# Optimization experiments

Measured on AMD Instinct MI355X. Metric: run time of the kernel, lower is better.

## Reference

```python
import jax, jax.numpy as jnp
import numpy as np

B, S, H, NH = 1, 4096, 768, 12
D = H // NH  # per-head dim = 64


def setup_inputs() -> dict:
    key = jax.random.key(0)
    ks = jax.random.split(key, 10)
    p = 0.02  # param scale
    return {
        "x": jax.random.normal(ks[0], (B, S, H), jnp.float32),
        "Wq": jax.random.normal(ks[1], (H, H), jnp.float32) * p,
        "bq": jax.random.normal(ks[2], (H,), jnp.float32) * p,
        "Wk": jax.random.normal(ks[3], (H, H), jnp.float32) * p,
        "bk": jax.random.normal(ks[4], (H,), jnp.float32) * p,
        "Wv": jax.random.normal(ks[5], (H, H), jnp.float32) * p,
        "bv": jax.random.normal(ks[6], (H,), jnp.float32) * p,
        "Wo": jax.random.normal(ks[7], (H, H), jnp.float32) * p,
        "bo": jax.random.normal(ks[8], (H,), jnp.float32) * p,
        "attn_mask": jax.random.randint(ks[9], (B, 1, 1, S), 0, 2).astype(bool),
    }


def _split_heads(t):
    # [B, S, H] -> [B, NH, S, D]
    return t.reshape(B, S, NH, D).transpose(0, 2, 1, 3)


def reference(x, Wq, bq, Wk, bk, Wv, bv, Wo, bo, attn_mask):
    q = _split_heads(x @ Wq.T + bq)
    k = _split_heads(x @ Wk.T + bk)
    v = _split_heads(x @ Wv.T + bv)
    scores = jnp.einsum('bhqd,bhkd->bhqk', q, k) / np.sqrt(D).astype(np.float32)
    scores = jnp.where(attn_mask, jnp.float32(-1e9), scores)
    attn = jax.nn.softmax(scores, axis=-1)
    ctx = jnp.einsum('bhqk,bhkd->bhqd', attn, v)
    ctx = ctx.transpose(0, 2, 1, 3).reshape(B, S, H)  # merge heads
    return ctx @ Wo.T + bo
```

## Files before the change

kernel.cpp:

```cpp
#include <hip/hip_runtime.h>
#include <stdint.h>

#define S_LEN 4096
#define HDIM  768
#define NHEAD 12
#define DHEAD 64

typedef _Float16 f16;
typedef __attribute__((ext_vector_type(8)))  _Float16 f16x8;
typedef __attribute__((ext_vector_type(4)))  _Float16 f16x4;
typedef __attribute__((ext_vector_type(4)))  float    f32x4;
typedef __attribute__((ext_vector_type(16))) float    f32x16;

typedef __attribute__((address_space(1))) void gv_t;
typedef __attribute__((address_space(3))) void lv_t;

__device__ __forceinline__ void async_copy16(const void* g, void* l) {
  __builtin_amdgcn_global_load_lds((gv_t*)g, (lv_t*)l, 16, 0, 0);
}

__device__ __forceinline__ float fast_exp2(float x) {
#if __has_builtin(__builtin_amdgcn_exp2f)
  return __builtin_amdgcn_exp2f(x);
#else
  return exp2f(x);
#endif
}

__device__ __forceinline__ int swz4(int row) { return (row ^ (row >> 2)) & 3; }

constexpr size_t OFF_META = 0;
constexpr size_t OFF_RIDX = 256;
constexpr size_t OFF_XB   = 65536;
constexpr size_t SZ_XB    = (size_t)S_LEN * HDIM * 2;
constexpr size_t OFF_WQKV = OFF_XB + SZ_XB;
constexpr size_t SZ_WQKV  = (size_t)3 * HDIM * HDIM * 2;
constexpr size_t OFF_WO   = OFF_WQKV + SZ_WQKV;
constexpr size_t SZ_WO    = (size_t)HDIM * HDIM * 2;
constexpr size_t OFF_Q    = OFF_WO + SZ_WO;
constexpr size_t SZ_HD    = (size_t)NHEAD * S_LEN * DHEAD * 2;
constexpr size_t OFF_K    = OFF_Q + SZ_HD;
constexpr size_t OFF_VT   = OFF_K + SZ_HD;
constexpr size_t OFF_VR   = OFF_VT + SZ_HD;
constexpr size_t OFF_PO1  = OFF_VR + SZ_HD;

__global__ __launch_bounds__(256) void k_prep(const float* __restrict__ x,
                                              const float* __restrict__ wq,
                                              const float* __restrict__ wk,
                                              const float* __restrict__ wv,
                                              const float* __restrict__ wo,
                                              const int* __restrict__ mi,
                                              f16* __restrict__ dst,
                                              int* __restrict__ ridx,
                                              int* __restrict__ meta) {
  __shared__ int s_flag;
  __shared__ int s_cnt[256];
  const int b = blockIdx.x, tid = threadIdx.x;
  if (b < 5376) {
    int i = b * 256 + tid;
    const float* src; int off;
    if (i < 786432) { src = x; off = i; }
    else {
      int j = i - 786432;
      int w = j / 147456;
      off = j - w * 147456;
      src = (w == 0) ? wq : (w == 1) ? wk : (w == 2) ? wv : wo;
    }
    float4 v = ((const float4*)src)[off];
    f16x4 h;
    h[0] = (f16)v.x; h[1] = (f16)v.y; h[2] = (f16)v.z; h[3] = (f16)v.w;
    ((f16x4*)dst)[i] = h;
    return;
  }
  if (tid == 0) s_flag = 1;
  __syncthreads();
  int bad = 0;
  #pragma unroll
  for (int k = 0; k < 4; ++k) {
    int v = mi[k * 256 + tid];
    if (v != 0 && v != 1) bad = 1;
  }
  if (bad) atomicAnd(&s_flag, 0);
  __syncthreads();
  const int isInt = s_flag;
  const unsigned char* mu8 = (const unsigned char*)mi;
  int keep[16]; int cnt = 0;
  const int s0 = tid * 16;
  #pragma unroll
  for (int k = 0; k < 16; ++k) {
    int mval = isInt ? mi[s0 + k] : (int)mu8[s0 + k];
    keep[k] = (mval == 0) ? 1 : 0;
    cnt += keep[k];
    ridx[s0 + k] = 0;
  }
  s_cnt[tid] = cnt;
  __syncthreads();
  for (int off = 1; off < 256; off <<= 1) {
    int t = (tid >= off) ? s_cnt[tid - off] : 0;
    __syncthreads();
    s_cnt[tid] += t;
    __syncthreads();
  }
  int base = s_cnt[tid] - cnt;
  #pragma unroll
  for (int k = 0; k < 16; ++k) {
    if (keep[k]) { ridx[base] = s0 + k; ++base; }
  }
  if (tid == 255) meta[0] = s_cnt[255];
}

__global__ __launch_bounds__(256) void k_qkv(
    const f16* __restrict__ xb, const f16* __restrict__ wqkv,
    const float* __restrict__ bq, const float* __restrict__ bk, const float* __restrict__ bv,
    const int* __restrict__ ridx, const int* __restrict__ meta,
    f16* __restrict__ Qh, f16* __restrict__ Kc, f16* __restrict__ Vrow) {
  __shared__ __attribute__((aligned(16))) f16 lA[128 * 32];
  __shared__ __attribute__((aligned(16))) f16 lB[128 * 32];
  const int tid = threadIdx.x;
  const int wid = tid >> 6, lane = tid & 63;
  const int hf = lane >> 5, l31 = lane & 31;
  const int wm = wid >> 1, wn = wid & 1;
  const int tn = blockIdx.x;
  const int m0 = blockIdx.y * 128;
  const int mat = tn / 6;
  const int nb = (tn % 6) * 128;
  const int kc = meta[0];
  if (mat != 0 && m0 >= kc) return;
  const f16* wbase = wqkv + (size_t)mat * HDIM * HDIM;

  const int ar0 = tid >> 2, ar1 = 64 + (tid >> 2);
  const f16* asrc0;
  const f16* asrc1;
  if (mat == 0) {
    asrc0 = xb + (size_t)(m0 + ar0) * HDIM;
    asrc1 = xb + (size_t)(m0 + ar1) * HDIM;
  } else {
    int g0 = (m0 + ar0 < kc) ? ridx[m0 + ar0] : 0;
    int g1 = (m0 + ar1 < kc) ? ridx[m0 + ar1] : 0;
    asrc0 = xb + (size_t)g0 * HDIM;
    asrc1 = xb + (size_t)g1 * HDIM;
  }
  const int slot = tid & 3;
  const int gs0 = slot ^ swz4(ar0);
  const int gs1 = slot ^ swz4(ar1);

  f32x16 acc[2][2] = {};

  for (int k0 = 0; k0 < HDIM; k0 += 32) {
    async_copy16((const char*)(asrc0 + k0) + gs0 * 16, (char*)lA + (wid * 64) * 16);
    async_copy16((const char*)(asrc1 + k0) + gs1 * 16, (char*)lA + (256 + wid * 64) * 16);
    async_copy16((const char*)(wbase + (size_t)(nb + ar0) * HDIM + k0) + gs0 * 16,
                 (char*)lB + (wid * 64) * 16);
    async_copy16((const char*)(wbase + (size_t)(nb + ar1) * HDIM + k0) + gs1 * 16,
                 (char*)lB + (256 + wid * 64) * 16);
    __syncthreads();
    #pragma unroll
    for (int kk = 0; kk < 2; ++kk) {
      f16x8 af[2], bf[2];
      #pragma unroll
      for (int mi = 0; mi < 2; ++mi) {
        int row = wm * 64 + mi * 32 + l31;
        af[mi] = *(const f16x8*)&lA[row * 32 + (((kk * 2 + hf) ^ swz4(row)) * 8)];
      }
      #pragma unroll
      for (int ni = 0; ni < 2; ++ni) {
        int row = wn * 64 + ni * 32 + l31;
        bf[ni] = *(const f16x8*)&lB[row * 32 + (((kk * 2 + hf) ^ swz4(row)) * 8)];
      }
      #pragma unroll
      for (int mi = 0; mi < 2; ++mi)
        #pragma unroll
        for (int ni = 0; ni < 2; ++ni)
          acc[mi][ni] = __builtin_amdgcn_mfma_f32_32x32x16_f16(af[mi], bf[ni], acc[mi][ni], 0, 0, 0);
    }
    __syncthreads();
  }

  const float* bias = (mat == 0) ? bq : (mat == 1) ? bk : bv;
  const float qscale = 0.125f * 1.44269504088896341f;
  f16* kvdst = (mat == 1) ? Kc : Vrow;
  #pragma unroll
  for (int mi = 0; mi < 2; ++mi) {
    #pragma unroll
    for (int ni = 0; ni < 2; ++ni) {
      int n = nb + wn * 64 + ni * 32 + l31;
      int head = n >> 6, d = n & 63;
      float b = bias[n];
      #pragma unroll
      for (int reg = 0; reg < 16; ++reg) {
        int s = m0 + wm * 64 + mi * 32 + (reg & 3) + 8 * (reg >> 2) + 4 * hf;
        float val = acc[mi][ni][reg] + b;
        if (mat == 0) {
          Qh[((size_t)head * S_LEN + s) * DHEAD + d] = (f16)(val * qscale);
        } else if (s < kc) {
          kvdst[((size_t)head * S_LEN + s) * DHEAD + d] = (f16)val;
        }
      }
    }
  }
}

__global__ __launch_bounds__(256) void k_vt(const int* __restrict__ meta,
                                            const f16* __restrict__ Vrow,
                                            f16* __restrict__ Vtc,
                                            f16* __restrict__ Kc) {
  const int kc = meta[0];
  const int kcp = (kc + 63) & ~63;
  const int p0 = blockIdx.x * 64;
  const int h = blockIdx.y;
  const int tid = threadIdx.x;
  if (p0 >= kcp) return;
  if (p0 <= kc && kc < p0 + 64 && kc < kcp) {
    const int npad = kcp - kc;
    for (int u = tid; u < npad * 8; u += 256) {
      int r = kc + (u >> 3), c8 = u & 7;
      f16x8 z = {};
      *(f16x8*)&Kc[((size_t)h * S_LEN + r) * DHEAD + c8 * 8] = z;
    }
  }
  __shared__ __attribute__((aligned(16))) f16 lT[64 * 80];
  for (int u = tid; u < 512; u += 256) {
    int d8 = u >> 6, p = u & 63;
    f16x8 v = {};
    if (p0 + p < kc) v = *(const f16x8*)&Vrow[((size_t)h * S_LEN + p0 + p) * DHEAD + d8 * 8];
    #pragma unroll
    for (int j = 0; j < 8; ++j) lT[(d8 * 8 + j) * 80 + p] = v[j];
  }
  __syncthreads();
  for (int w = tid; w < 512; w += 256) {
    int d = w >> 3, p8 = w & 7;
    int base16 = (p8 >> 1) * 16, half = p8 & 1;
    f16x4 lo = *(const f16x4*)&lT[d * 80 + base16 + half * 4];
    f16x4 hi = *(const f16x4*)&lT[d * 80 + base16 + 8 + half * 4];
    f16x8 o;
    o[0] = lo[0]; o[1] = lo[1]; o[2] = lo[2]; o[3] = lo[3];
    o[4] = hi[0]; o[5] = hi[1]; o[6] = hi[2]; o[7] = hi[3];
    *(f16x8*)&Vtc[((size_t)h * DHEAD + d) * S_LEN + p0 + p8 * 8] = o;
  }
}

__global__ __launch_bounds__(256, 3) void k_attn(
    const f16* __restrict__ Qh, const f16* __restrict__ Kc, const f16* __restrict__ Vtc,
    const int* __restrict__ meta, f16* __restrict__ PO0, f16* __restrict__ PO1,
    float* __restrict__ PL) {
  __shared__ __attribute__((aligned(16))) f16 lK[64 * 64];
  __shared__ __attribute__((aligned(16))) f16 lV[64 * 64];
  const int tid = threadIdx.x;
  const int wid = tid >> 6, lane = tid & 63;
  const int hf = lane >> 5, l31 = lane & 31, r7 = l31 & 7;
  const int head = blockIdx.y;
  const int split = blockIdx.z;
  const int q0 = blockIdx.x * 128 + wid * 32;
  const int kc = meta[0];
  const int nkt = (kc + 63) >> 6;
  const int th = nkt >> 1;
  const int t0 = split ? th : 0;
  const int t1 = split ? nkt : th;

  const f16* Qp = Qh + ((size_t)head * S_LEN + q0 + l31) * DHEAD;
  f16x8 qf[4];
  #pragma unroll
  for (int dc = 0; dc < 4; ++dc) qf[dc] = *(const f16x8*)(Qp + dc * 16 + hf * 8);

  f32x16 accO[2] = {};
  float lsum = 0.f;

  const char* kbase = (const char*)(Kc + (size_t)head * S_LEN * DHEAD);
  const char* vbase = (const char*)(Vtc + (size_t)head * DHEAD * S_LEN);

  for (int t = t0; t < t1; ++t) {
    const int j0 = t * 64;
    #pragma unroll
    for (int iss = 0; iss < 2; ++iss) {
      int c = iss * 256 + tid;
      int row = c >> 3, slot = c & 7;
      int gs = slot ^ (row & 7);
      async_copy16(kbase + (size_t)(j0 + row) * 128 + gs * 16,
                   (char*)lK + (iss * 256 + wid * 64) * 16);
      async_copy16(vbase + (size_t)row * (S_LEN * 2) + (size_t)j0 * 2 + gs * 16,
                   (char*)lV + (iss * 256 + wid * 64) * 16);
    }
    __syncthreads();

    #pragma unroll
    for (int mh = 0; mh < 2; ++mh) {
      f16x8 af[4];
      const int arow = mh * 32 + l31;
      #pragma unroll
      for (int dc = 0; dc < 4; ++dc)
        af[dc] = *(const f16x8*)&lK[arow * 64 + ((((dc << 1) | hf) ^ r7) * 8)];
      f32x16 s = {};
      #pragma unroll
      for (int dc = 0; dc < 4; ++dc)
        s = __builtin_amdgcn_mfma_f32_32x32x16_f16(af[dc], qf[dc], s, 0, 0, 0);
      #pragma unroll
      for (int u = 0; u < 16; ++u) { s[u] = fast_exp2(s[u]); lsum += s[u]; }
      #pragma unroll
      for (int cc = 0; cc < 2; ++cc) {
        f16x8 pf;
        #pragma unroll
        for (int u = 0; u < 8; ++u) pf[u] = (f16)s[8 * cc + u];
        const int c2 = mh * 2 + cc;
        #pragma unroll
        for (int dh = 0; dh < 2; ++dh) {
          const int vrow = dh * 32 + l31;
          f16x8 vf = *(const f16x8*)&lV[vrow * 64 + ((((c2 << 1) | hf) ^ r7) * 8)];
          accO[dh] = __builtin_amdgcn_mfma_f32_32x32x16_f16(pf, vf, accO[dh], 0, 0, 0);
        }
      }
    }
    __syncthreads();
  }

  lsum += __shfl_xor(lsum, 32);
  if (split == 1) lsum -= (float)(nkt * 64 - kc);
  if (hf == 0)
    PL[((size_t)split * NHEAD + head) * S_LEN + q0 + l31] = lsum;

  f16* PO = split ? PO1 : PO0;
  #pragma unroll
  for (int dh = 0; dh < 2; ++dh)
    #pragma unroll
    for (int reg = 0; reg < 16; ++reg) {
      int row = (reg & 3) + 8 * (reg >> 2) + 4 * hf;
      PO[((size_t)head * S_LEN + q0 + row) * DHEAD + dh * 32 + l31] = (f16)accO[dh][reg];
    }
}

__global__ __launch_bounds__(256) void k_out(
    const f16* __restrict__ PO0, const f16* __restrict__ PO1,
    const float* __restrict__ PL, const f16* __restrict__ wo,
    const float* __restrict__ bo, float* __restrict__ out) {
  __shared__ __attribute__((aligned(16))) f16 lA[128 * 32];
  __shared__ __attribute__((aligned(16))) f16 lB[128 * 32];
  __shared__ float linv[NHEAD * 128];
  const int tid = threadIdx.x;
  const int wid = tid >> 6, lane = tid & 63;
  const int hf = lane >> 5, l31 = lane & 31;
  const int wm = wid >> 1, wn = wid & 1;
  const int nb = blockIdx.x * 128;
  const int m0 = blockIdx.y * 128;

  for (int i = tid; i < NHEAD * 128; i += 256) {
    int h = i >> 7, r = i & 127;
    float l = PL[(size_t)h * S_LEN + m0 + r] + PL[(size_t)(NHEAD + h) * S_LEN + m0 + r];
    linv[i] = 1.0f / l;
  }
  __syncthreads();

  f32x16 acc[2][2] = {};

  for (int k0 = 0; k0 < HDIM; k0 += 32) {
    const int head = k0 >> 6, d0 = k0 & 63;
    #pragma unroll
    for (int iss = 0; iss < 2; ++iss) {
      int c = iss * 256 + tid;
      int row = c >> 2, slot = c & 3;
      int gs = slot ^ swz4(row);
      size_t pi = ((size_t)head * S_LEN + m0 + row) * DHEAD + d0 + gs * 8;
      f16x8 a0 = *(const f16x8*)(PO0 + pi);
      f16x8 a1 = *(const f16x8*)(PO1 + pi);
      float il = linv[head * 128 + row];
      f16x8 av;
      #pragma unroll
      for (int u = 0; u < 8; ++u) av[u] = (f16)(((float)a0[u] + (float)a1[u]) * il);
      *(f16x8*)&lA[c * 8] = av;
      async_copy16((const char*)(wo + (size_t)(nb + row) * HDIM + k0) + gs * 16,
                   (char*)lB + (iss * 256 + wid * 64) * 16);
    }
    __syncthreads();
    #pragma unroll
    for (int kk = 0; kk < 2; ++kk) {
      f16x8 af[2], bf[2];
      #pragma unroll
      for (int mi = 0; mi < 2; ++mi) {
        int row = wm * 64 + mi * 32 + l31;
        af[mi] = *(const f16x8*)&lA[row * 32 + (((kk * 2 + hf) ^ swz4(row)) * 8)];
      }
      #pragma unroll
      for (int ni = 0; ni < 2; ++ni) {
        int row = wn * 64 + ni * 32 + l31;
        bf[ni] = *(const f16x8*)&lB[row * 32 + (((kk * 2 + hf) ^ swz4(row)) * 8)];
      }
      #pragma unroll
      for (int mi = 0; mi < 2; ++mi)
        #pragma unroll
        for (int ni = 0; ni < 2; ++ni)
          acc[mi][ni] = __builtin_amdgcn_mfma_f32_32x32x16_f16(af[mi], bf[ni], acc[mi][ni], 0, 0, 0);
    }
    __syncthreads();
  }

  #pragma unroll
  for (int mi = 0; mi < 2; ++mi) {
    #pragma unroll
    for (int ni = 0; ni < 2; ++ni) {
      int n = nb + wn * 64 + ni * 32 + l31;
      float b = bo[n];
      #pragma unroll
      for (int reg = 0; reg < 16; ++reg) {
        int s = m0 + wm * 64 + mi * 32 + (reg & 3) + 8 * (reg >> 2) + 4 * hf;
        out[(size_t)s * HDIM + n] = acc[mi][ni][reg] + b;
      }
    }
  }
}

extern "C" void kernel_launch(void* const* d_in, const int* in_sizes, int n_in,
                              void* d_out, int out_size, void* d_ws, size_t ws_size,
                              hipStream_t stream) {
  const float* x  = (const float*)d_in[0];
  const float* Wq = (const float*)d_in[1];
  const float* bq = (const float*)d_in[2];
  const float* Wk = (const float*)d_in[3];
  const float* bk = (const float*)d_in[4];
  const float* Wv = (const float*)d_in[5];
  const float* bv = (const float*)d_in[6];
  const float* Wo = (const float*)d_in[7];
  const float* bo = (const float*)d_in[8];
  const int*   mask = (const int*)d_in[9];
  float* out = (float*)d_out;

  char* ws = (char*)d_ws;
  int* meta  = (int*)(ws + OFF_META);
  int* ridx  = (int*)(ws + OFF_RIDX);
  f16* xb    = (f16*)(ws + OFF_XB);
  f16* wqkv  = (f16*)(ws + OFF_WQKV);
  f16* wob   = (f16*)(ws + OFF_WO);
  f16* Qh    = (f16*)(ws + OFF_Q);
  f16* Kc    = (f16*)(ws + OFF_K);
  f16* Vtc   = (f16*)(ws + OFF_VT);
  f16* Vrow  = (f16*)(ws + OFF_VR);
  f16* PO0   = (f16*)(ws + OFF_VR);
  f16* PO1   = (f16*)(ws + OFF_PO1);
  float* PL  = (float*)(ws + OFF_WQKV);

  k_prep<<<dim3(5377), 256, 0, stream>>>(x, Wq, Wk, Wv, Wo, mask, xb, ridx, meta);
  k_qkv<<<dim3(18, 32), 256, 0, stream>>>(xb, wqkv, bq, bk, bv, ridx, meta, Qh, Kc, Vrow);
  k_vt<<<dim3(64, NHEAD), 256, 0, stream>>>(meta, Vrow, Vtc, Kc);
  k_attn<<<dim3(32, NHEAD, 2), 256, 0, stream>>>(Qh, Kc, Vtc, meta, PO0, PO1, PL);
  k_out<<<dim3(6, 32), 256, 0, stream>>>(PO0, PO1, PL, wob, bo, out);
}
```

Measured before the change: 182.9 us.

## Double-buffer K/V tiles in attention and remap blocks per XCD

The attention kernel now keeps two LDS buffers for K and V and issues the async load of the next key tile before computing on the current one. This lets global-to-LDS copies overlap with MFMA work and drops one barrier per iteration. The 3D grid is flattened to 1D with a remap that keeps blocks of the same head and split on the same XCD, for better L2 reuse of K/V. The softmax row sum is split into four partial accumulators to shorten the dependency chain. LDS use doubles, which may lower occupancy.

```diff
diff --git a/kernel.cpp b/kernel.cpp
--- a/kernel.cpp
+++ b/kernel.cpp
@@ -243,14 +243,19 @@
     const f16* __restrict__ Qh, const f16* __restrict__ Kc, const f16* __restrict__ Vtc,
     const int* __restrict__ meta, f16* __restrict__ PO0, f16* __restrict__ PO1,
     float* __restrict__ PL) {
-  __shared__ __attribute__((aligned(16))) f16 lK[64 * 64];
-  __shared__ __attribute__((aligned(16))) f16 lV[64 * 64];
+  __shared__ __attribute__((aligned(16))) f16 lK[2][64 * 64];
+  __shared__ __attribute__((aligned(16))) f16 lV[2][64 * 64];
   const int tid = threadIdx.x;
   const int wid = tid >> 6, lane = tid & 63;
   const int hf = lane >> 5, l31 = lane & 31, r7 = l31 & 7;
-  const int head = blockIdx.y;
-  const int split = blockIdx.z;
-  const int q0 = blockIdx.x * 128 + wid * 32;
+
+  const int lid = blockIdx.x;
+  const int w = ((lid & 7) * 96) + (lid >> 3);
+  const int head = w >> 6;
+  const int rem = w & 63;
+  const int split = rem >> 5;
+  const int q0 = (rem & 31) * 128 + wid * 32;
+
   const int kc = meta[0];
   const int nkt = (kc + 63) >> 6;
   const int th = nkt >> 1;
@@ -263,24 +268,37 @@
   for (int dc = 0; dc < 4; ++dc) qf[dc] = *(const f16x8*)(Qp + dc * 16 + hf * 8);
 
   f32x16 accO[2] = {};
-  float lsum = 0.f;
+  float ls0 = 0.f, ls1 = 0.f, ls2 = 0.f, ls3 = 0.f;
 
   const char* kbase = (const char*)(Kc + (size_t)head * S_LEN * DHEAD);
   const char* vbase = (const char*)(Vtc + (size_t)head * DHEAD * S_LEN);
 
+  const int c0row = tid >> 3,        c0slot = tid & 7;
+  const int c1row = (256 + tid) >> 3, c1slot = tid & 7;
+  const int gs0 = c0slot ^ (c0row & 7);
+  const int gs1 = c1slot ^ (c1row & 7);
+
+  auto stage = [&](int t, int buf) {
+    const int j0 = t * 64;
+    async_copy16(kbase + (size_t)(j0 + c0row) * 128 + gs0 * 16,
+                 (char*)&lK[buf][0] + (wid * 64) * 16);
+    async_copy16(vbase + (size_t)c0row * (S_LEN * 2) + (size_t)j0 * 2 + gs0 * 16,
+                 (char*)&lV[buf][0] + (wid * 64) * 16);
+    async_copy16(kbase + (size_t)(j0 + c1row) * 128 + gs1 * 16,
+                 (char*)&lK[buf][0] + (256 + wid * 64) * 16);
+    async_copy16(vbase + (size_t)c1row * (S_LEN * 2) + (size_t)j0 * 2 + gs1 * 16,
+                 (char*)&lV[buf][0] + (256 + wid * 64) * 16);
+  };
+
+  int cur = 0;
+  if (t0 < t1) {
+    stage(t0, 0);
+    __syncthreads();
+  }
+
   for (int t = t0; t < t1; ++t) {
-    const int j0 = t * 64;
-    #pragma unroll
-    for (int iss = 0; iss < 2; ++iss) {
-      int c = iss * 256 + tid;
-      int row = c >> 3, slot = c & 7;
-      int gs = slot ^ (row & 7);
-      async_copy16(kbase + (size_t)(j0 + row) * 128 + gs * 16,
-                   (char*)lK + (iss * 256 + wid * 64) * 16);
-      async_copy16(vbase + (size_t)row * (S_LEN * 2) + (size_t)j0 * 2 + gs * 16,
-                   (char*)lV + (iss * 256 + wid * 64) * 16);
-    }
-    __syncthreads();
+    const bool more = (t + 1 < t1);
+    if (more) stage(t + 1, cur ^ 1);
 
     #pragma unroll
     for (int mh = 0; mh < 2; ++mh) {
@@ -288,13 +306,19 @@
       const int arow = mh * 32 + l31;
       #pragma unroll
       for (int dc = 0; dc < 4; ++dc)
-        af[dc] = *(const f16x8*)&lK[arow * 64 + ((((dc << 1) | hf) ^ r7) * 8)];
+        af[dc] = *(const f16x8*)&lK[cur][arow * 64 + ((((dc << 1) | hf) ^ r7) * 8)];
       f32x16 s = {};
       #pragma unroll
       for (int dc = 0; dc < 4; ++dc)
         s = __builtin_amdgcn_mfma_f32_32x32x16_f16(af[dc], qf[dc], s, 0, 0, 0);
       #pragma unroll
-      for (int u = 0; u < 16; ++u) { s[u] = fast_exp2(s[u]); lsum += s[u]; }
+      for (int u = 0; u < 16; ++u) {
+        s[u] = fast_exp2(s[u]);
+        if ((u & 3) == 0) ls0 += s[u];
+        else if ((u & 3) == 1) ls1 += s[u];
+        else if ((u & 3) == 2) ls2 += s[u];
+        else ls3 += s[u];
+      }
       #pragma unroll
       for (int cc = 0; cc < 2; ++cc) {
         f16x8 pf;
@@ -304,14 +328,19 @@
         #pragma unroll
         for (int dh = 0; dh < 2; ++dh) {
           const int vrow = dh * 32 + l31;
-          f16x8 vf = *(const f16x8*)&lV[vrow * 64 + ((((c2 << 1) | hf) ^ r7) * 8)];
+          f16x8 vf = *(const f16x8*)&lV[cur][vrow * 64 + ((((c2 << 1) | hf) ^ r7) * 8)];
           accO[dh] = __builtin_amdgcn_mfma_f32_32x32x16_f16(pf, vf, accO[dh], 0, 0, 0);
         }
       }
     }
-    __syncthreads();
-  }
-
+
+    if (more) {
+      __syncthreads();
+      cur ^= 1;
+    }
+  }
+
+  float lsum = (ls0 + ls1) + (ls2 + ls3);
   lsum += __shfl_xor(lsum, 32);
   if (split == 1) lsum -= (float)(nkt * 64 - kc);
   if (hf == 0)
@@ -438,6 +467,6 @@
   k_prep<<<dim3(5377), 256, 0, stream>>>(x, Wq, Wk, Wv, Wo, mask, xb, ridx, meta);
   k_qkv<<<dim3(18, 32), 256, 0, stream>>>(xb, wqkv, bq, bk, bv, ridx, meta, Qh, Kc, Vrow);
   k_vt<<<dim3(64, NHEAD), 256, 0, stream>>>(meta, Vrow, Vtc, Kc);
-  k_attn<<<dim3(32, NHEAD, 2), 256, 0, stream>>>(Qh, Kc, Vtc, meta, PO0, PO1, PL);
+  k_attn<<<dim3(768), 256, 0, stream>>>(Qh, Kc, Vtc, meta, PO0, PO1, PL);
   k_out<<<dim3(6, 32), 256, 0, stream>>>(PO0, PO1, PL, wob, bo, out);
 }
```

Result: faster. 178.2 us (-2.6%).
